# Optimization experiments

Measured on AMD Instinct MI355X. Metric: run time of the kernel, lower is better.

The kernel has to match this reference:

```python
import jax, jax.numpy as jnp
import numpy as np

S, B, I, H, O = 512, 256, 64, 512, 25

def setup_inputs() -> dict:
    key = jax.random.key(0)
    ks = jax.random.split(key, 7)
    k = 1.0 / np.sqrt(H)  # torch nn.RNN / nn.Linear default init bound
    x = jax.random.normal(ks[0], (S, B, I), dtype=jnp.float32)
    W_ih = jax.random.uniform(ks[1], (H, I), jnp.float32, -k, k)
    W_hh = jax.random.uniform(ks[2], (H, H), jnp.float32, -k, k)
    b_ih = jax.random.uniform(ks[3], (H,), jnp.float32, -k, k)
    b_hh = jax.random.uniform(ks[4], (H,), jnp.float32, -k, k)
    W2 = jax.random.uniform(ks[5], (O, H), jnp.float32, -k, k)
    b2 = jax.random.uniform(ks[6], (O,), jnp.float32, -k, k)
    return {"x": x, "W_ih": W_ih, "W_hh": W_hh, "b_ih": b_ih, "b_hh": b_hh, "W2": W2, "b2": b2}

def reference(x, W_ih, W_hh, b_ih, b_hh, W2, b2):
    # Precompute input projection for all timesteps in one big GEMM: (S,B,H)
    xi = jnp.einsum('sbi,hi->sbh', x, W_ih) + b_ih
    h0 = jnp.zeros((x.shape[1], W_hh.shape[0]), dtype=x.dtype)
    W_hh_T = W_hh.T
    def step(h_prev, xi_t):
        h = jax.nn.relu(xi_t + h_prev @ W_hh_T + b_hh)
        return h, h
    _, out = jax.lax.scan(step, h0, xi)  # out: (S, B, H)
    # Faithful to original: out[:, -1, :] selects last batch element -> (S, H)
    y = out[:, -1, :] @ W2.T + b2  # (S, 25)
    return y
```

## Files before the change

### kernel.cpp

```cpp
#include <hip/hip_runtime.h>


#define S_ 512
#define B_ 256
#define I_ 64
#define H_ 512
#define O_ 25
#define G_ 16
#define R_ 32

__global__ __launch_bounds__(256) void rnn_pre(
    const float* __restrict__ x, const float* __restrict__ W_ih,
    const float* __restrict__ b_ih, const float* __restrict__ b_hh,
    float* __restrict__ xi, unsigned* __restrict__ hg) {
  const int t = blockIdx.x;
  const int tid = threadIdx.x;
  const int o = blockIdx.y * 256 + tid;
  if (t == 0 && blockIdx.y == 0) {
    hg[tid] = 0x80000000u;
    hg[tid + 256] = 0x80000000u;
    hg[tid + 512] = 0x80000000u;
    hg[tid + 768] = 0x80000000u;
  }
  __shared__ float xr[I_];
  if (tid < I_) xr[tid] = x[(t * B_ + (B_ - 1)) * I_ + tid];
  __syncthreads();
  float acc = b_ih[o] + b_hh[o];
  const float4* wp = (const float4*)(W_ih + o * I_);
#pragma unroll
  for (int j = 0; j < I_ / 4; ++j) {
    float4 w4 = wp[j];
    acc += w4.x * xr[4 * j] + w4.y * xr[4 * j + 1] + w4.z * xr[4 * j + 2] +
           w4.w * xr[4 * j + 3];
  }
  xi[t * H_ + o] = acc;
}

__global__ __launch_bounds__(256) void rnn_seq(
    const float* __restrict__ W_hh, const float* __restrict__ xi,
    float* __restrict__ hseq, unsigned* __restrict__ hg) {
  const int tid = threadIdx.x;
  const int b = blockIdx.x;
  const int r = tid & 31;
  const int seg = tid >> 5;
  const int row = b * R_ + r;
  const int k0 = seg * 64;
  const int wave = tid >> 6;
  const int own_lo = b * R_;
  const int own_hi = b * R_ + R_;

  __shared__ float h_l[H_];
  __shared__ float part[4 * R_];

  float w[64];
  {
    const float4* wp = (const float4*)(W_hh + row * H_ + k0);
#pragma unroll
    for (int j = 0; j < 16; ++j) {
      float4 v = wp[j];
      w[4 * j] = v.x; w[4 * j + 1] = v.y; w[4 * j + 2] = v.z; w[4 * j + 3] = v.w;
    }
  }
  for (int n = tid; n < H_; n += 256) h_l[n] = 0.0f;

  float xiv = (tid < R_) ? xi[own_lo + tid] : 0.0f;
  __syncthreads();

  const int n0 = tid, n1 = tid + 256;
  const bool own0 = (n0 >= own_lo && n0 < own_hi);
  const bool own1 = (n1 >= own_lo && n1 < own_hi);

  for (int s = 0; s < S_; ++s) {
    float a0 = 0.f, a1 = 0.f, a2 = 0.f, a3 = 0.f;
    const float4* hp = (const float4*)(h_l + k0);
#pragma unroll
    for (int j = 0; j < 16; ++j) {
      float4 hv = hp[j];
      a0 = fmaf(w[4 * j + 0], hv.x, a0);
      a1 = fmaf(w[4 * j + 1], hv.y, a1);
      a2 = fmaf(w[4 * j + 2], hv.z, a2);
      a3 = fmaf(w[4 * j + 3], hv.w, a3);
    }
    float acc = (a0 + a1) + (a2 + a3);
    acc += __shfl_xor(acc, 32, 64);
    if ((tid & 32) == 0) part[wave * R_ + r] = acc;
    __syncthreads();

    const unsigned phase = (unsigned)((s >> 1) & 1);
    unsigned* buf = hg + (s & 1) * H_;

    if (tid < R_) {
      float sum = part[tid] + part[R_ + tid] + part[2 * R_ + tid] +
                  part[3 * R_ + tid] + xiv;
      float h = fmaxf(sum, 0.0f);
      h_l[own_lo + tid] = h;
      hseq[s * H_ + own_lo + tid] = h;
      __hip_atomic_store(&buf[own_lo + tid],
                         __float_as_uint(h) | (phase << 31),
                         __ATOMIC_RELAXED, __HIP_MEMORY_SCOPE_AGENT);
    }

    if (s == S_ - 1) break;

    if (tid < R_) xiv = xi[(s + 1) * H_ + own_lo + tid];

    bool need0 = !own0, need1 = !own1;
    unsigned p0, p1;
    while (need0 | need1) {
      if (need0)
        p0 = __hip_atomic_load(&buf[n0], __ATOMIC_RELAXED, __HIP_MEMORY_SCOPE_AGENT);
      if (need1)
        p1 = __hip_atomic_load(&buf[n1], __ATOMIC_RELAXED, __HIP_MEMORY_SCOPE_AGENT);
      if (need0 && (p0 >> 31) == phase) {
        h_l[n0] = __uint_as_float(p0 & 0x7fffffffu);
        need0 = false;
      }
      if (need1 && (p1 >> 31) == phase) {
        h_l[n1] = __uint_as_float(p1 & 0x7fffffffu);
        need1 = false;
      }
    }
    __syncthreads();
  }
}

__global__ __launch_bounds__(256) void rnn_post(
    const float* __restrict__ hseq, const float* __restrict__ W2,
    const float* __restrict__ b2, float* __restrict__ y) {
  const int t = blockIdx.x;
  const int tid = threadIdx.x;
  __shared__ float hl[H_];
  __shared__ float part[256];
  for (int n = tid; n < H_; n += 256) hl[n] = hseq[t * H_ + n];
  __syncthreads();
  const int o = tid >> 3;
  const int seg = tid & 7;
  float acc = 0.0f;
  if (o < O_) {
    const float4* wp = (const float4*)(W2 + o * H_ + seg * 64);
    const float4* hp = (const float4*)(hl + seg * 64);
#pragma unroll
    for (int j = 0; j < 16; ++j) {
      float4 w4 = wp[j];
      float4 h4 = hp[j];
      acc += w4.x * h4.x + w4.y * h4.y + w4.z * h4.z + w4.w * h4.w;
    }
  }
  part[tid] = acc;
  __syncthreads();
  if (tid < O_) {
    float sum = 0.0f;
#pragma unroll
    for (int j = 0; j < 8; ++j) sum += part[tid * 8 + j];
    y[t * O_ + tid] = sum + b2[tid];
  }
}

extern "C" void kernel_launch(void* const* d_in, const int* in_sizes, int n_in,
                              void* d_out, int out_size, void* d_ws, size_t ws_size,
                              hipStream_t stream) {
  const float* x    = (const float*)d_in[0];
  const float* W_ih = (const float*)d_in[1];
  const float* W_hh = (const float*)d_in[2];
  const float* b_ih = (const float*)d_in[3];
  const float* b_hh = (const float*)d_in[4];
  const float* W2   = (const float*)d_in[5];
  const float* b2   = (const float*)d_in[6];
  float* y = (float*)d_out;

  float* xi   = (float*)d_ws;
  float* hseq = xi + S_ * H_;
  unsigned* hg = (unsigned*)(hseq + S_ * H_);

  rnn_pre<<<dim3(S_, 2), 256, 0, stream>>>(x, W_ih, b_ih, b_hh, xi, hg);
  rnn_seq<<<G_, 256, 0, stream>>>(W_hh, xi, hseq, hg);
  rnn_post<<<S_, 256, 0, stream>>>(hseq, W2, b2, y);
}
```

Measured before the change: 787.5 us.

## Restructure recurrent kernel to 64 single-wave blocks with register-resident hidden state

The sequential RNN kernel now uses 64 blocks of one 64-lane wave each. Every block owns 8 hidden rows and every lane holds an 8x8 weight tile in registers. Lanes poll four 64-bit flagged words straight from the global exchange buffer into registers, and the reduction uses wave shuffles, so shared memory and __syncthreads are gone from the per-step loop. The hidden output overwrites the xi buffer in place, which drops one workspace array. In exchange the cross-block sync now spans 64 blocks instead of 16, and every lane spins on global atomics.

```diff
diff --git a/kernel.cpp b/kernel.cpp
--- a/kernel.cpp
+++ b/kernel.cpp
@@ -6,13 +6,13 @@
 #define I_ 64
 #define H_ 512
 #define O_ 25
-#define G_ 16
-#define R_ 32
+#define NB_ 64
+#define RW_ 8
 
 __global__ __launch_bounds__(256) void rnn_pre(
     const float* __restrict__ x, const float* __restrict__ W_ih,
     const float* __restrict__ b_ih, const float* __restrict__ b_hh,
-    float* __restrict__ xi, unsigned* __restrict__ hg) {
+    float* __restrict__ xh, unsigned* __restrict__ hg) {
   const int t = blockIdx.x;
   const int tid = threadIdx.x;
   const int o = blockIdx.y * 256 + tid;
@@ -33,94 +33,104 @@
     acc += w4.x * xr[4 * j] + w4.y * xr[4 * j + 1] + w4.z * xr[4 * j + 2] +
            w4.w * xr[4 * j + 3];
   }
-  xi[t * H_ + o] = acc;
+  xh[t * H_ + o] = acc;
 }
 
-__global__ __launch_bounds__(256) void rnn_seq(
-    const float* __restrict__ W_hh, const float* __restrict__ xi,
-    float* __restrict__ hseq, unsigned* __restrict__ hg) {
-  const int tid = threadIdx.x;
+__global__ __launch_bounds__(64) void rnn_seq(
+    const float* __restrict__ W_hh, float* __restrict__ xh,
+    unsigned* hg) {
+  const int l = threadIdx.x;
   const int b = blockIdx.x;
-  const int r = tid & 31;
-  const int seg = tid >> 5;
-  const int row = b * R_ + r;
-  const int k0 = seg * 64;
-  const int wave = tid >> 6;
-  const int own_lo = b * R_;
-  const int own_hi = b * R_ + R_;
+  const int own_lo = b * RW_;
+  const int k0 = l * RW_;
 
-  __shared__ float h_l[H_];
-  __shared__ float part[4 * R_];
+  float w[RW_][RW_];
+#pragma unroll
+  for (int r = 0; r < RW_; ++r) {
+    const float4* wp = (const float4*)(W_hh + (own_lo + r) * H_ + k0);
+    float4 wa = wp[0], wb = wp[1];
+    w[r][0] = wa.x; w[r][1] = wa.y; w[r][2] = wa.z; w[r][3] = wa.w;
+    w[r][4] = wb.x; w[r][5] = wb.y; w[r][6] = wb.z; w[r][7] = wb.w;
+  }
 
-  float w[64];
-  {
-    const float4* wp = (const float4*)(W_hh + row * H_ + k0);
+  float h[RW_];
 #pragma unroll
-    for (int j = 0; j < 16; ++j) {
-      float4 v = wp[j];
-      w[4 * j] = v.x; w[4 * j + 1] = v.y; w[4 * j + 2] = v.z; w[4 * j + 3] = v.w;
-    }
-  }
-  for (int n = tid; n < H_; n += 256) h_l[n] = 0.0f;
+  for (int j = 0; j < RW_; ++j) h[j] = 0.0f;
 
-  float xiv = (tid < R_) ? xi[own_lo + tid] : 0.0f;
-  __syncthreads();
+  float xiv = (l < RW_) ? xh[own_lo + l] : 0.0f;
 
-  const int n0 = tid, n1 = tid + 256;
-  const bool own0 = (n0 >= own_lo && n0 < own_hi);
-  const bool own1 = (n1 >= own_lo && n1 < own_hi);
+  const unsigned long long sm = 0x8000000080000000ull;
 
   for (int s = 0; s < S_; ++s) {
-    float a0 = 0.f, a1 = 0.f, a2 = 0.f, a3 = 0.f;
-    const float4* hp = (const float4*)(h_l + k0);
+    float acc[RW_];
 #pragma unroll
-    for (int j = 0; j < 16; ++j) {
-      float4 hv = hp[j];
-      a0 = fmaf(w[4 * j + 0], hv.x, a0);
-      a1 = fmaf(w[4 * j + 1], hv.y, a1);
-      a2 = fmaf(w[4 * j + 2], hv.z, a2);
-      a3 = fmaf(w[4 * j + 3], hv.w, a3);
+    for (int r = 0; r < RW_; ++r) {
+      float a = w[r][0] * h[0];
+      a = fmaf(w[r][1], h[1], a);
+      a = fmaf(w[r][2], h[2], a);
+      a = fmaf(w[r][3], h[3], a);
+      a = fmaf(w[r][4], h[4], a);
+      a = fmaf(w[r][5], h[5], a);
+      a = fmaf(w[r][6], h[6], a);
+      a = fmaf(w[r][7], h[7], a);
+      acc[r] = a;
     }
-    float acc = (a0 + a1) + (a2 + a3);
-    acc += __shfl_xor(acc, 32, 64);
-    if ((tid & 32) == 0) part[wave * R_ + r] = acc;
-    __syncthreads();
+
+    float s4[4];
+#pragma unroll
+    for (int i = 0; i < 4; ++i) {
+      float e = acc[2 * i] + __shfl_xor(acc[2 * i], 1);
+      float o2 = acc[2 * i + 1] + __shfl_xor(acc[2 * i + 1], 1);
+      s4[i] = (l & 1) ? o2 : e;
+    }
+    float s2[2];
+#pragma unroll
+    for (int i = 0; i < 2; ++i) {
+      float e = s4[2 * i] + __shfl_xor(s4[2 * i], 2);
+      float o2 = s4[2 * i + 1] + __shfl_xor(s4[2 * i + 1], 2);
+      s2[i] = (l & 2) ? o2 : e;
+    }
+    float e = s2[0] + __shfl_xor(s2[0], 4);
+    float o2 = s2[1] + __shfl_xor(s2[1], 4);
+    float v = (l & 4) ? o2 : e;
+    v += __shfl_xor(v, 8);
+    v += __shfl_xor(v, 16);
+    v += __shfl_xor(v, 32);
 
     const unsigned phase = (unsigned)((s >> 1) & 1);
     unsigned* buf = hg + (s & 1) * H_;
 
-    if (tid < R_) {
-      float sum = part[tid] + part[R_ + tid] + part[2 * R_ + tid] +
-                  part[3 * R_ + tid] + xiv;
-      float h = fmaxf(sum, 0.0f);
-      h_l[own_lo + tid] = h;
-      hseq[s * H_ + own_lo + tid] = h;
-      __hip_atomic_store(&buf[own_lo + tid],
-                         __float_as_uint(h) | (phase << 31),
+    if (l < RW_) {
+      float hv = fmaxf(v + xiv, 0.0f);
+      xh[s * H_ + own_lo + l] = hv;
+      __hip_atomic_store(buf + own_lo + l,
+                         __float_as_uint(hv) | (phase << 31),
                          __ATOMIC_RELAXED, __HIP_MEMORY_SCOPE_AGENT);
     }
 
     if (s == S_ - 1) break;
 
-    if (tid < R_) xiv = xi[(s + 1) * H_ + own_lo + tid];
+    if (l < RW_) xiv = xh[(s + 1) * H_ + own_lo + l];
 
-    bool need0 = !own0, need1 = !own1;
-    unsigned p0, p1;
-    while (need0 | need1) {
-      if (need0)
-        p0 = __hip_atomic_load(&buf[n0], __ATOMIC_RELAXED, __HIP_MEMORY_SCOPE_AGENT);
-      if (need1)
-        p1 = __hip_atomic_load(&buf[n1], __ATOMIC_RELAXED, __HIP_MEMORY_SCOPE_AGENT);
-      if (need0 && (p0 >> 31) == phase) {
-        h_l[n0] = __uint_as_float(p0 & 0x7fffffffu);
-        need0 = false;
-      }
-      if (need1 && (p1 >> 31) == phase) {
-        h_l[n1] = __uint_as_float(p1 & 0x7fffffffu);
-        need1 = false;
-      }
+    const unsigned long long ph64 = phase ? sm : 0ull;
+    const unsigned long long* ap = (const unsigned long long*)(buf + k0);
+    unsigned long long p0, p1, p2, p3;
+    for (;;) {
+      p0 = __hip_atomic_load(ap + 0, __ATOMIC_RELAXED, __HIP_MEMORY_SCOPE_AGENT);
+      p1 = __hip_atomic_load(ap + 1, __ATOMIC_RELAXED, __HIP_MEMORY_SCOPE_AGENT);
+      p2 = __hip_atomic_load(ap + 2, __ATOMIC_RELAXED, __HIP_MEMORY_SCOPE_AGENT);
+      p3 = __hip_atomic_load(ap + 3, __ATOMIC_RELAXED, __HIP_MEMORY_SCOPE_AGENT);
+      unsigned long long t = (p0 ^ ph64) | (p1 ^ ph64) | (p2 ^ ph64) | (p3 ^ ph64);
+      if ((t & sm) == 0ull) break;
     }
-    __syncthreads();
+    h[0] = __uint_as_float((unsigned)p0 & 0x7fffffffu);
+    h[1] = __uint_as_float((unsigned)(p0 >> 32) & 0x7fffffffu);
+    h[2] = __uint_as_float((unsigned)p1 & 0x7fffffffu);
+    h[3] = __uint_as_float((unsigned)(p1 >> 32) & 0x7fffffffu);
+    h[4] = __uint_as_float((unsigned)p2 & 0x7fffffffu);
+    h[5] = __uint_as_float((unsigned)(p2 >> 32) & 0x7fffffffu);
+    h[6] = __uint_as_float((unsigned)p3 & 0x7fffffffu);
+    h[7] = __uint_as_float((unsigned)(p3 >> 32) & 0x7fffffffu);
   }
 }
 
@@ -168,11 +178,10 @@
   const float* b2   = (const float*)d_in[6];
   float* y = (float*)d_out;
 
-  float* xi   = (float*)d_ws;
-  float* hseq = xi + S_ * H_;
-  unsigned* hg = (unsigned*)(hseq + S_ * H_);
+  float* xh = (float*)d_ws;
+  unsigned* hg = (unsigned*)(xh + S_ * H_);
 
-  rnn_pre<<<dim3(S_, 2), 256, 0, stream>>>(x, W_ih, b_ih, b_hh, xi, hg);
-  rnn_seq<<<G_, 256, 0, stream>>>(W_hh, xi, hseq, hg);
-  rnn_post<<<S_, 256, 0, stream>>>(hseq, W2, b2, y);
+  rnn_pre<<<dim3(S_, 2), 256, 0, stream>>>(x, W_ih, b_ih, b_hh, xh, hg);
+  rnn_seq<<<NB_, 64, 0, stream>>>(W_hh, xh, hg);
+  rnn_post<<<S_, 256, 0, stream>>>(xh, W2, b2, y);
 }
```

Result: slower. 889.5 us (+13.0%).

## Halve cross-block sync fan-in with 8 larger blocks and 64-bit flag polling

Applied to the files above, without the earlier changes.

Restructures the sequential RNN kernel from 16 blocks of 256 threads to 8 blocks of 512 threads, each owning 64 hidden rows, so fewer blocks take part in the per-timestep global handshake. The flagged hidden values are now published and polled as 64-bit pairs by 256 dedicated threads, which replaces the old shuffle-plus-partial reduction and the per-element polling loop. The hidden sequence overwrites the xi buffer in place, removing a separate workspace array. The trade-off is less parallelism per step across the device and a larger intra-block reduction, in return for lower synchronization latency on each step.

```diff
diff --git a/kernel.cpp b/kernel.cpp
--- a/kernel.cpp
+++ b/kernel.cpp
@@ -6,13 +6,13 @@
 #define I_ 64
 #define H_ 512
 #define O_ 25
-#define G_ 16
-#define R_ 32
+#define NB_ 8
+#define RB_ 64
 
 __global__ __launch_bounds__(256) void rnn_pre(
     const float* __restrict__ x, const float* __restrict__ W_ih,
     const float* __restrict__ b_ih, const float* __restrict__ b_hh,
-    float* __restrict__ xi, unsigned* __restrict__ hg) {
+    float* __restrict__ xh, unsigned* __restrict__ hg) {
   const int t = blockIdx.x;
   const int tid = threadIdx.x;
   const int o = blockIdx.y * 256 + tid;
@@ -33,24 +33,23 @@
     acc += w4.x * xr[4 * j] + w4.y * xr[4 * j + 1] + w4.z * xr[4 * j + 2] +
            w4.w * xr[4 * j + 3];
   }
-  xi[t * H_ + o] = acc;
+  xh[t * H_ + o] = acc;
 }
 
-__global__ __launch_bounds__(256) void rnn_seq(
-    const float* __restrict__ W_hh, const float* __restrict__ xi,
-    float* __restrict__ hseq, unsigned* __restrict__ hg) {
+__global__ __launch_bounds__(512) void rnn_seq(
+    const float* __restrict__ W_hh, float* __restrict__ xh,
+    unsigned* hg) {
   const int tid = threadIdx.x;
   const int b = blockIdx.x;
-  const int r = tid & 31;
-  const int seg = tid >> 5;
-  const int row = b * R_ + r;
+  const int r = tid & 63;
+  const int seg = tid >> 6;
+  const int row = b * RB_ + r;
   const int k0 = seg * 64;
-  const int wave = tid >> 6;
-  const int own_lo = b * R_;
-  const int own_hi = b * R_ + R_;
+  const int own_lo = b * RB_;
+  const int lane = tid & 63;
 
-  __shared__ float h_l[H_];
-  __shared__ float part[4 * R_];
+  __shared__ __align__(16) float h_l[H_];
+  __shared__ __align__(16) float part[8 * 64];
 
   float w[64];
   {
@@ -58,17 +57,21 @@
 #pragma unroll
     for (int j = 0; j < 16; ++j) {
       float4 v = wp[j];
-      w[4 * j] = v.x; w[4 * j + 1] = v.y; w[4 * j + 2] = v.z; w[4 * j + 3] = v.w;
+      w[4 * j] = v.x; w[4 * j + 1] = v.y;
+      w[4 * j + 2] = v.z; w[4 * j + 3] = v.w;
     }
   }
-  for (int n = tid; n < H_; n += 256) h_l[n] = 0.0f;
+  for (int n = tid; n < H_; n += 512) h_l[n] = 0.0f;
 
-  float xiv = (tid < R_) ? xi[own_lo + tid] : 0.0f;
+  const bool fin = (tid < 32);
+  float2 xiv = make_float2(0.f, 0.f);
+  if (fin) xiv = *(const float2*)(xh + own_lo + 2 * tid);
+
+  const bool pol = (tid >= 128) && (tid < 384);
+  const int p = tid - 128;
+
+  const unsigned long long sm = 0x8000000080000000ull;
   __syncthreads();
-
-  const int n0 = tid, n1 = tid + 256;
-  const bool own0 = (n0 >= own_lo && n0 < own_hi);
-  const bool own1 = (n1 >= own_lo && n1 < own_hi);
 
   for (int s = 0; s < S_; ++s) {
     float a0 = 0.f, a1 = 0.f, a2 = 0.f, a3 = 0.f;
@@ -81,44 +84,54 @@
       a2 = fmaf(w[4 * j + 2], hv.z, a2);
       a3 = fmaf(w[4 * j + 3], hv.w, a3);
     }
-    float acc = (a0 + a1) + (a2 + a3);
-    acc += __shfl_xor(acc, 32, 64);
-    if ((tid & 32) == 0) part[wave * R_ + r] = acc;
+    part[seg * 64 + r] = (a0 + a1) + (a2 + a3);
     __syncthreads();
 
     const unsigned phase = (unsigned)((s >> 1) & 1);
     unsigned* buf = hg + (s & 1) * H_;
 
-    if (tid < R_) {
-      float sum = part[tid] + part[R_ + tid] + part[2 * R_ + tid] +
-                  part[3 * R_ + tid] + xiv;
-      float h = fmaxf(sum, 0.0f);
-      h_l[own_lo + tid] = h;
-      hseq[s * H_ + own_lo + tid] = h;
-      __hip_atomic_store(&buf[own_lo + tid],
-                         __float_as_uint(h) | (phase << 31),
+    if (fin) {
+      const int j = tid;
+      const float2* pp = (const float2*)part;
+      float sx = xiv.x, sy = xiv.y;
+#pragma unroll
+      for (int q = 0; q < 8; ++q) {
+        float2 f = pp[q * 32 + j];
+        sx += f.x;
+        sy += f.y;
+      }
+      float h0 = fmaxf(sx, 0.0f);
+      float h1 = fmaxf(sy, 0.0f);
+      *(float2*)(xh + s * H_ + own_lo + 2 * j) = make_float2(h0, h1);
+      unsigned long long uv =
+          (unsigned long long)(__float_as_uint(h0) | (phase << 31)) |
+          ((unsigned long long)(__float_as_uint(h1) | (phase << 31)) << 32);
+      __hip_atomic_store((unsigned long long*)(buf + own_lo + 2 * j), uv,
                          __ATOMIC_RELAXED, __HIP_MEMORY_SCOPE_AGENT);
     }
 
     if (s == S_ - 1) break;
 
-    if (tid < R_) xiv = xi[(s + 1) * H_ + own_lo + tid];
+    if (fin) xiv = *(const float2*)(xh + (s + 1) * H_ + own_lo + 2 * tid);
 
-    bool need0 = !own0, need1 = !own1;
-    unsigned p0, p1;
-    while (need0 | need1) {
-      if (need0)
-        p0 = __hip_atomic_load(&buf[n0], __ATOMIC_RELAXED, __HIP_MEMORY_SCOPE_AGENT);
-      if (need1)
-        p1 = __hip_atomic_load(&buf[n1], __ATOMIC_RELAXED, __HIP_MEMORY_SCOPE_AGENT);
-      if (need0 && (p0 >> 31) == phase) {
-        h_l[n0] = __uint_as_float(p0 & 0x7fffffffu);
-        need0 = false;
+    if (pol) {
+      const unsigned long long ph64 = phase ? sm : 0ull;
+      const unsigned long long* ap =
+          (const unsigned long long*)buf + p;
+      unsigned long long va = __hip_atomic_load(ap, __ATOMIC_RELAXED,
+                                                __HIP_MEMORY_SCOPE_AGENT);
+      unsigned long long vb = __hip_atomic_load(ap, __ATOMIC_RELAXED,
+                                                __HIP_MEMORY_SCOPE_AGENT);
+      for (;;) {
+        if (((va ^ ph64) & sm) == 0ull) break;
+        va = vb;
+        vb = __hip_atomic_load(ap, __ATOMIC_RELAXED,
+                               __HIP_MEMORY_SCOPE_AGENT);
       }
-      if (need1 && (p1 >> 31) == phase) {
-        h_l[n1] = __uint_as_float(p1 & 0x7fffffffu);
-        need1 = false;
-      }
+      float2 hv;
+      hv.x = __uint_as_float((unsigned)va & 0x7fffffffu);
+      hv.y = __uint_as_float((unsigned)(va >> 32) & 0x7fffffffu);
+      *(float2*)(h_l + 2 * p) = hv;
     }
     __syncthreads();
   }
@@ -168,11 +181,10 @@
   const float* b2   = (const float*)d_in[6];
   float* y = (float*)d_out;
 
-  float* xi   = (float*)d_ws;
-  float* hseq = xi + S_ * H_;
-  unsigned* hg = (unsigned*)(hseq + S_ * H_);
+  float* xh = (float*)d_ws;
+  unsigned* hg = (unsigned*)(xh + S_ * H_);
 
-  rnn_pre<<<dim3(S_, 2), 256, 0, stream>>>(x, W_ih, b_ih, b_hh, xi, hg);
-  rnn_seq<<<G_, 256, 0, stream>>>(W_hh, xi, hseq, hg);
-  rnn_post<<<S_, 256, 0, stream>>>(hseq, W2, b2, y);
+  rnn_pre<<<dim3(S_, 2), 256, 0, stream>>>(x, W_ih, b_ih, b_hh, xh, hg);
+  rnn_seq<<<NB_, 512, 0, stream>>>(W_hh, xh, hg);
+  rnn_post<<<S_, 256, 0, stream>>>(xh, W2, b2, y);
 }
```

After: 875.0 us. +11.1%, slower.

## Poll hidden state with 64-bit loads, adaptive backoff, and lightweight LDS barriers

Applied to the files above, without the earlier changes.

The cross-block spin-wait now has each non-owning thread poll one 64-bit pair of flagged hidden values instead of two 32-bit slots. It adds an adaptive s_sleep backoff to reduce polling traffic on the shared buffer, and replaces __syncthreads with a raw s_barrier that waits only on lgkmcnt. The hidden sequence overwrites the xi buffer in place to drop one workspace array, and partial sums are laid out so a single float4 read gathers them. The risks are extra latency from the backoff delay and reliance on the weaker barrier being correct for the LDS and global accesses involved.

```diff
diff --git a/kernel.cpp b/kernel.cpp
--- a/kernel.cpp
+++ b/kernel.cpp
@@ -9,10 +9,17 @@
 #define G_ 16
 #define R_ 32
 
+static __device__ __forceinline__ void wg_barrier_lds() {
+  __builtin_amdgcn_sched_barrier(0);
+  asm volatile("s_waitcnt lgkmcnt(0)" ::: "memory");
+  __builtin_amdgcn_s_barrier();
+  __builtin_amdgcn_sched_barrier(0);
+}
+
 __global__ __launch_bounds__(256) void rnn_pre(
     const float* __restrict__ x, const float* __restrict__ W_ih,
     const float* __restrict__ b_ih, const float* __restrict__ b_hh,
-    float* __restrict__ xi, unsigned* __restrict__ hg) {
+    float* __restrict__ xh, unsigned* __restrict__ hg) {
   const int t = blockIdx.x;
   const int tid = threadIdx.x;
   const int o = blockIdx.y * 256 + tid;
@@ -33,12 +40,12 @@
     acc += w4.x * xr[4 * j] + w4.y * xr[4 * j + 1] + w4.z * xr[4 * j + 2] +
            w4.w * xr[4 * j + 3];
   }
-  xi[t * H_ + o] = acc;
+  xh[t * H_ + o] = acc;
 }
 
 __global__ __launch_bounds__(256) void rnn_seq(
-    const float* __restrict__ W_hh, const float* __restrict__ xi,
-    float* __restrict__ hseq, unsigned* __restrict__ hg) {
+    const float* __restrict__ W_hh, float* __restrict__ xh,
+    unsigned* hg) {
   const int tid = threadIdx.x;
   const int b = blockIdx.x;
   const int r = tid & 31;
@@ -47,10 +54,9 @@
   const int k0 = seg * 64;
   const int wave = tid >> 6;
   const int own_lo = b * R_;
-  const int own_hi = b * R_ + R_;
 
-  __shared__ float h_l[H_];
-  __shared__ float part[4 * R_];
+  __shared__ __align__(16) float h_l[H_];
+  __shared__ __align__(16) float part[R_ * 4];
 
   float w[64];
   {
@@ -58,17 +64,18 @@
 #pragma unroll
     for (int j = 0; j < 16; ++j) {
       float4 v = wp[j];
-      w[4 * j] = v.x; w[4 * j + 1] = v.y; w[4 * j + 2] = v.z; w[4 * j + 3] = v.w;
+      w[4 * j] = v.x; w[4 * j + 1] = v.y;
+      w[4 * j + 2] = v.z; w[4 * j + 3] = v.w;
     }
   }
   for (int n = tid; n < H_; n += 256) h_l[n] = 0.0f;
 
-  float xiv = (tid < R_) ? xi[own_lo + tid] : 0.0f;
-  __syncthreads();
+  float xiv = (tid < R_) ? xh[own_lo + tid] : 0.0f;
+  wg_barrier_lds();
 
-  const int n0 = tid, n1 = tid + 256;
-  const bool own0 = (n0 >= own_lo && n0 < own_hi);
-  const bool own1 = (n1 >= own_lo && n1 < own_hi);
+  const bool ownp = (tid >= b * (R_ / 2)) && (tid < (b + 1) * (R_ / 2));
+  const unsigned long long sm = 0x8000000080000000ull;
+  int D = 0;
 
   for (int s = 0; s < S_; ++s) {
     float a0 = 0.f, a1 = 0.f, a2 = 0.f, a3 = 0.f;
@@ -83,44 +90,49 @@
     }
     float acc = (a0 + a1) + (a2 + a3);
     acc += __shfl_xor(acc, 32, 64);
-    if ((tid & 32) == 0) part[wave * R_ + r] = acc;
-    __syncthreads();
+    if ((tid & 32) == 0) part[r * 4 + wave] = acc;
+    wg_barrier_lds();
 
     const unsigned phase = (unsigned)((s >> 1) & 1);
     unsigned* buf = hg + (s & 1) * H_;
 
     if (tid < R_) {
-      float sum = part[tid] + part[R_ + tid] + part[2 * R_ + tid] +
-                  part[3 * R_ + tid] + xiv;
+      float4 p4 = *(const float4*)(part + tid * 4);
+      float sum = p4.x + p4.y + p4.z + p4.w + xiv;
       float h = fmaxf(sum, 0.0f);
-      h_l[own_lo + tid] = h;
-      hseq[s * H_ + own_lo + tid] = h;
       __hip_atomic_store(&buf[own_lo + tid],
                          __float_as_uint(h) | (phase << 31),
                          __ATOMIC_RELAXED, __HIP_MEMORY_SCOPE_AGENT);
+      h_l[own_lo + tid] = h;
+      xh[s * H_ + own_lo + tid] = h;
     }
 
     if (s == S_ - 1) break;
 
-    if (tid < R_) xiv = xi[(s + 1) * H_ + own_lo + tid];
+    if (tid < R_) xiv = xh[(s + 1) * H_ + own_lo + tid];
 
-    bool need0 = !own0, need1 = !own1;
-    unsigned p0, p1;
-    while (need0 | need1) {
-      if (need0)
-        p0 = __hip_atomic_load(&buf[n0], __ATOMIC_RELAXED, __HIP_MEMORY_SCOPE_AGENT);
-      if (need1)
-        p1 = __hip_atomic_load(&buf[n1], __ATOMIC_RELAXED, __HIP_MEMORY_SCOPE_AGENT);
-      if (need0 && (p0 >> 31) == phase) {
-        h_l[n0] = __uint_as_float(p0 & 0x7fffffffu);
-        need0 = false;
-      }
-      if (need1 && (p1 >> 31) == phase) {
-        h_l[n1] = __uint_as_float(p1 & 0x7fffffffu);
-        need1 = false;
+    if (!ownp) {
+      for (int d = 0; d < D; ++d) __builtin_amdgcn_s_sleep(1);
+      const unsigned long long ph64 = phase ? sm : 0ull;
+      const unsigned long long* ap = (const unsigned long long*)buf + tid;
+      unsigned long long v;
+      int n = 0;
+      do {
+        v = __hip_atomic_load(ap, __ATOMIC_RELAXED, __HIP_MEMORY_SCOPE_AGENT);
+        ++n;
+      } while (((v ^ ph64) & sm) != 0ull);
+      float2 hv;
+      hv.x = __uint_as_float((unsigned)v & 0x7fffffffu);
+      hv.y = __uint_as_float((unsigned)(v >> 32) & 0x7fffffffu);
+      *(float2*)(h_l + 2 * tid) = hv;
+      if (n > 1) {
+        D += (n - 1);
+        if (D > 40) D = 40;
+      } else if ((s & 7) == 0 && D > 0) {
+        --D;
       }
     }
-    __syncthreads();
+    wg_barrier_lds();
   }
 }
 
@@ -168,11 +180,10 @@
   const float* b2   = (const float*)d_in[6];
   float* y = (float*)d_out;
 
-  float* xi   = (float*)d_ws;
-  float* hseq = xi + S_ * H_;
-  unsigned* hg = (unsigned*)(hseq + S_ * H_);
+  float* xh = (float*)d_ws;
+  unsigned* hg = (unsigned*)(xh + S_ * H_);
 
-  rnn_pre<<<dim3(S_, 2), 256, 0, stream>>>(x, W_ih, b_ih, b_hh, xi, hg);
-  rnn_seq<<<G_, 256, 0, stream>>>(W_hh, xi, hseq, hg);
-  rnn_post<<<S_, 256, 0, stream>>>(hseq, W2, b2, y);
+  rnn_pre<<<dim3(S_, 2), 256, 0, stream>>>(x, W_ih, b_ih, b_hh, xh, hg);
+  rnn_seq<<<G_, 256, 0, stream>>>(W_hh, xh, hg);
+  rnn_post<<<S_, 256, 0, stream>>>(xh, W2, b2, y);
 }
```

After: 753.3 us. 1.05x faster.
